# Kernel tuning notes

Hardware: AMD Instinct MI355X
Metric: run time of the kernel (lower is better)

## Reference

```python
import jax, jax.numpy as jnp
import numpy as np

N_NODES = 50000


def gcn_conv(x, row, col, W, b, n_nodes):
    # x: [N, Cin], row/col: [E+N] (self-loops already appended)
    x = x @ W  # [N, Cout]
    deg = jax.ops.segment_sum(jnp.ones(col.shape, x.dtype), col, num_segments=n_nodes)
    dinv = jnp.where(deg > 0, jax.lax.rsqrt(deg), 0.0)
    norm = dinv[row] * dinv[col]  # [E+N]
    msgs = x[row] * norm[:, None]  # gather + scale, [E+N, Cout]
    out = jax.ops.segment_sum(msgs, col, num_segments=n_nodes)
    return out + b


def setup_inputs() -> dict:
    key = jax.random.key(0)
    ks = jax.random.split(key, 5)
    n, e = N_NODES, 640000
    d_in, d_h, d_out = 128, 128, 64
    x = jax.random.normal(ks[0], (n, d_in), dtype=jnp.float32)
    edge_index = jax.random.randint(ks[1], (2, e), 0, n, dtype=jnp.int64)
    s1 = 1.0 / np.sqrt(d_in)
    s2 = 1.0 / np.sqrt(d_h)
    W1 = jax.random.normal(ks[2], (d_in, d_h), dtype=jnp.float32) * s1
    W2 = jax.random.normal(ks[3], (d_h, d_h), dtype=jnp.float32) * s2
    Wl = jax.random.normal(ks[4], (d_h, d_out), dtype=jnp.float32) * s2
    return {
        "x": x, "edge_index": edge_index,
        "W1": W1, "b1": jnp.zeros((d_h,), jnp.float32),
        "W2": W2, "b2": jnp.zeros((d_h,), jnp.float32),
        "Wl": Wl, "bl": jnp.zeros((d_out,), jnp.float32),
    }


def reference(x, edge_index, W1, b1, W2, b2, Wl, bl):
    n = x.shape[0]
    loops = jnp.arange(n, dtype=edge_index.dtype)
    row = jnp.concatenate([edge_index[0], loops])  # add self-loops (PyG GCNConv)
    col = jnp.concatenate([edge_index[1], loops])
    h = jax.nn.relu(gcn_conv(x, row, col, W1, b1, n))  # dropout is identity in eval
    h = jax.nn.relu(gcn_conv(h, row, col, W2, b2, n))
    return h @ Wl + bl
```

## Files before the change

### kernel.cpp

```cpp
#include <hip/hip_runtime.h>
#include <hip/hip_fp16.h>

#define NN 50000
#define NE 640000
#define RB ((NN + 255) / 256)

#define SC_GROUPS 8
#define SC_RANGE (NN / SC_GROUPS)
#define SC_EPT 8
#define SC_CHUNK (256 * SC_EPT)
#define SC_CHUNKS ((NE + SC_CHUNK - 1) / SC_CHUNK)

struct __align__(8) edge_t { int r; float w; };

__device__ __forceinline__ int edge_at(const void* p, long long i, int m64) {
    if (m64) return (int)((const long long*)p)[i];
    return ((const int*)p)[i];
}

__device__ __forceinline__ int detect_m64(const unsigned* w, int tid) {
    __shared__ int found;
    if (tid == 0) found = 0;
    __syncthreads();
    if (tid < 256 && w[2 * tid + 1] != 0u) atomicAdd(&found, 1);
    __syncthreads();
    return (found == 0) ? 1 : 0;
}

__global__ __launch_bounds__(256) void k_count(const void* __restrict__ e,
                                               int* __restrict__ deg) {
    int m = detect_m64((const unsigned*)e, threadIdx.x);
    int i = blockIdx.x * 256 + threadIdx.x;
    if (i >= NE) return;
    int c = edge_at(e, (long long)NE + i, m);
    if ((unsigned)c < (unsigned)NN) atomicAdd(&deg[c], 1);
}

__global__ __launch_bounds__(256) void k_reduce(const int* __restrict__ deg,
                                                int* __restrict__ bsum) {
    __shared__ int s[256];
    int i = blockIdx.x * 256 + threadIdx.x;
    s[threadIdx.x] = (i < NN) ? deg[i] : 0;
    __syncthreads();
    for (int d = 128; d > 0; d >>= 1) {
        if (threadIdx.x < d) s[threadIdx.x] += s[threadIdx.x + d];
        __syncthreads();
    }
    if (threadIdx.x == 0) bsum[blockIdx.x] = s[0];
}

__global__ __launch_bounds__(256) void k_apply(const int* __restrict__ deg,
                                               const int* __restrict__ bsum,
                                               int* __restrict__ offs,
                                               int* __restrict__ cursor,
                                               float* __restrict__ dinv) {
    __shared__ int s[256];
    __shared__ int base_s;
    int t = threadIdx.x;
    int v = (t < RB && t < blockIdx.x) ? bsum[t] : 0;
    s[t] = v;
    __syncthreads();
    for (int d = 128; d > 0; d >>= 1) {
        if (t < d) s[t] += s[t + d];
        __syncthreads();
    }
    if (t == 0) base_s = s[0];
    __syncthreads();
    int base = base_s;
    __syncthreads();
    int i = blockIdx.x * 256 + t;
    int dg = (i < NN) ? deg[i] : 0;
    s[t] = dg;
    __syncthreads();
    for (int d = 1; d < 256; d <<= 1) {
        int u = (t >= d) ? s[t - d] : 0;
        __syncthreads();
        s[t] += u;
        __syncthreads();
    }
    if (i < NN) {
        int excl = base + s[t] - dg;
        offs[i] = excl;
        cursor[i] = excl;
        dinv[i] = rsqrtf((float)(dg + 1));
        if (i == NN - 1) offs[NN] = excl + dg;
    }
}

__global__ __launch_bounds__(256) void k_scatter(const void* __restrict__ e,
                                                 int* __restrict__ cursor,
                                                 edge_t* __restrict__ ew,
                                                 const float* __restrict__ dinv) {
    int m = detect_m64((const unsigned*)e, threadIdx.x);
    int b = blockIdx.x;
    int g = b & (SC_GROUPS - 1);
    int chunk = b >> 3;
    int clo = g * SC_RANGE, chi = clo + SC_RANGE;
    int base = chunk * SC_CHUNK + threadIdx.x;
#pragma unroll
    for (int j = 0; j < SC_EPT; j++) {
        int i = base + j * 256;
        if (i < NE) {
            int c = edge_at(e, (long long)NE + i, m);
            if (c >= clo && c < chi) {
                int r = edge_at(e, (long long)i, m);
                r = min(max(r, 0), NN - 1);
                int p = atomicAdd(&cursor[c], 1);
                edge_t t2; t2.r = r; t2.w = dinv[r];
                ew[p] = t2;
            }
        }
    }
}

__global__ __launch_bounds__(256) void k_gemm128h(const float* __restrict__ A,
                                                  const float* __restrict__ W,
                                                  __half* __restrict__ Th) {
    __shared__ float Ws[64 * 128];
    int t = threadIdx.x;
    int rg = t >> 4, cg = t & 15;
    int row0 = blockIdx.x * 32 + rg * 2;
    const float4* a0 = (const float4*)(A + (long long)min(row0 + 0, NN - 1) * 128);
    const float4* a1 = (const float4*)(A + (long long)min(row0 + 1, NN - 1) * 128);
    float acc[2][8];
#pragma unroll
    for (int i = 0; i < 2; i++)
#pragma unroll
        for (int j = 0; j < 8; j++) acc[i][j] = 0.f;
#pragma unroll
    for (int h = 0; h < 2; h++) {
        __syncthreads();
#pragma unroll
        for (int i = 0; i < 8; i++)
            ((float4*)Ws)[t + 256 * i] = ((const float4*)(W + h * 64 * 128))[t + 256 * i];
        __syncthreads();
#pragma unroll 4
        for (int k4 = 0; k4 < 16; k4++) {
            float4 av0 = a0[h * 16 + k4];
            float4 av1 = a1[h * 16 + k4];
#pragma unroll
            for (int kk = 0; kk < 4; kk++) {
                float4 w0 = *(const float4*)&Ws[(k4 * 4 + kk) * 128 + cg * 4];
                float4 w1 = *(const float4*)&Ws[(k4 * 4 + kk) * 128 + cg * 4 + 64];
                float x0 = (kk == 0) ? av0.x : (kk == 1) ? av0.y : (kk == 2) ? av0.z : av0.w;
                float x1 = (kk == 0) ? av1.x : (kk == 1) ? av1.y : (kk == 2) ? av1.z : av1.w;
                acc[0][0] += x0 * w0.x; acc[0][1] += x0 * w0.y;
                acc[0][2] += x0 * w0.z; acc[0][3] += x0 * w0.w;
                acc[0][4] += x0 * w1.x; acc[0][5] += x0 * w1.y;
                acc[0][6] += x0 * w1.z; acc[0][7] += x0 * w1.w;
                acc[1][0] += x1 * w0.x; acc[1][1] += x1 * w0.y;
                acc[1][2] += x1 * w0.z; acc[1][3] += x1 * w0.w;
                acc[1][4] += x1 * w1.x; acc[1][5] += x1 * w1.y;
                acc[1][6] += x1 * w1.z; acc[1][7] += x1 * w1.w;
            }
        }
    }
#pragma unroll
    for (int i = 0; i < 2; i++) {
        int row = row0 + i;
        if (row < NN) {
            __half2 p0 = __floats2half2_rn(acc[i][0], acc[i][1]);
            __half2 p1 = __floats2half2_rn(acc[i][2], acc[i][3]);
            __half2 p2 = __floats2half2_rn(acc[i][4], acc[i][5]);
            __half2 p3 = __floats2half2_rn(acc[i][6], acc[i][7]);
            uint2 u0; u0.x = *(unsigned*)&p0; u0.y = *(unsigned*)&p1;
            uint2 u1; u1.x = *(unsigned*)&p2; u1.y = *(unsigned*)&p3;
            *(uint2*)(Th + (long long)row * 128 + cg * 4) = u0;
            *(uint2*)(Th + (long long)row * 128 + cg * 4 + 64) = u1;
        }
    }
}

__global__ __launch_bounds__(256) void k_gemm64(const float* __restrict__ A,
                                                const float* __restrict__ W,
                                                const float* __restrict__ b,
                                                float* __restrict__ T) {
    __shared__ float Ws[128 * 64];
    int t = threadIdx.x;
#pragma unroll
    for (int i = 0; i < 8; i++)
        ((float4*)Ws)[t + 256 * i] = ((const float4*)W)[t + 256 * i];
    __syncthreads();
    int rg = t >> 4, cg = t & 15;
    int row0 = blockIdx.x * 32 + rg * 2;
    const float4* a0 = (const float4*)(A + (long long)min(row0 + 0, NN - 1) * 128);
    const float4* a1 = (const float4*)(A + (long long)min(row0 + 1, NN - 1) * 128);
    float acc[2][4];
#pragma unroll
    for (int i = 0; i < 2; i++)
#pragma unroll
        for (int j = 0; j < 4; j++) acc[i][j] = 0.f;
#pragma unroll 4
    for (int k4 = 0; k4 < 32; k4++) {
        float4 av0 = a0[k4];
        float4 av1 = a1[k4];
#pragma unroll
        for (int kk = 0; kk < 4; kk++) {
            float4 w = *(const float4*)&Ws[(k4 * 4 + kk) * 64 + cg * 4];
            float x0 = (kk == 0) ? av0.x : (kk == 1) ? av0.y : (kk == 2) ? av0.z : av0.w;
            float x1 = (kk == 0) ? av1.x : (kk == 1) ? av1.y : (kk == 2) ? av1.z : av1.w;
            acc[0][0] += x0 * w.x; acc[0][1] += x0 * w.y;
            acc[0][2] += x0 * w.z; acc[0][3] += x0 * w.w;
            acc[1][0] += x1 * w.x; acc[1][1] += x1 * w.y;
            acc[1][2] += x1 * w.z; acc[1][3] += x1 * w.w;
        }
    }
    float4 bb = ((const float4*)b)[cg];
#pragma unroll
    for (int i = 0; i < 2; i++) {
        int row = row0 + i;
        if (row < NN) {
            float4 v = {acc[i][0] + bb.x, acc[i][1] + bb.y,
                        acc[i][2] + bb.z, acc[i][3] + bb.w};
            *(float4*)&T[(long long)row * 64 + cg * 4] = v;
        }
    }
}

__device__ __forceinline__ float4 h4_to_f4(uint2 u) {
    __half2 h0 = *reinterpret_cast<const __half2*>(&u.x);
    __half2 h1 = *reinterpret_cast<const __half2*>(&u.y);
    float2 f0 = __half22float2(h0);
    float2 f1 = __half22float2(h1);
    float4 r; r.x = f0.x; r.y = f0.y; r.z = f1.x; r.w = f1.y;
    return r;
}

__global__ __launch_bounds__(256) void k_agg_h(const __half* __restrict__ X,
                                               const int* __restrict__ offs,
                                               const edge_t* __restrict__ ew,
                                               const float* __restrict__ dinv,
                                               const float* __restrict__ b,
                                               float* __restrict__ H) {
    int t = threadIdx.x;
    int node = blockIdx.x * 4 + (t >> 6);
    if (node >= NN) return;
    int lane = t & 63;
    int half = lane >> 5;
    int l32 = lane & 31;
    const uint2* X2 = (const uint2*)X;
    float dc = dinv[node];
    float4 acc = {0.f, 0.f, 0.f, 0.f};
    if (half == 0) {
        float4 s = h4_to_f4(X2[(long long)node * 32 + l32]);
        acc.x = dc * s.x; acc.y = dc * s.y; acc.z = dc * s.z; acc.w = dc * s.w;
    }
    int e0 = offs[node], e1 = offs[node + 1];
    int n = e1 - e0;
    const edge_t* ep = ew + e0;
    int i = half;
    for (; i + 6 < n; i += 8) {
        edge_t m0 = ep[i], m1 = ep[i + 2], m2 = ep[i + 4], m3 = ep[i + 6];
        uint2 u0 = X2[(long long)m0.r * 32 + l32];
        uint2 u1 = X2[(long long)m1.r * 32 + l32];
        uint2 u2 = X2[(long long)m2.r * 32 + l32];
        uint2 u3 = X2[(long long)m3.r * 32 + l32];
        float4 v0 = h4_to_f4(u0), v1 = h4_to_f4(u1);
        float4 v2 = h4_to_f4(u2), v3 = h4_to_f4(u3);
        acc.x += m0.w * v0.x + m1.w * v1.x + m2.w * v2.x + m3.w * v3.x;
        acc.y += m0.w * v0.y + m1.w * v1.y + m2.w * v2.y + m3.w * v3.y;
        acc.z += m0.w * v0.z + m1.w * v1.z + m2.w * v2.z + m3.w * v3.z;
        acc.w += m0.w * v0.w + m1.w * v1.w + m2.w * v2.w + m3.w * v3.w;
    }
    for (; i < n; i += 2) {
        edge_t m = ep[i];
        float4 v = h4_to_f4(X2[(long long)m.r * 32 + l32]);
        acc.x += m.w * v.x; acc.y += m.w * v.y;
        acc.z += m.w * v.z; acc.w += m.w * v.w;
    }
    float4 oth;
    oth.x = __shfl_xor(acc.x, 32);
    oth.y = __shfl_xor(acc.y, 32);
    oth.z = __shfl_xor(acc.z, 32);
    oth.w = __shfl_xor(acc.w, 32);
    float4 bb = ((const float4*)b)[l32];
    float4 o;
    o.x = fmaxf(dc * (acc.x + oth.x) + bb.x, 0.f);
    o.y = fmaxf(dc * (acc.y + oth.y) + bb.y, 0.f);
    o.z = fmaxf(dc * (acc.z + oth.z) + bb.z, 0.f);
    o.w = fmaxf(dc * (acc.w + oth.w) + bb.w, 0.f);
    if (half == 0)
        ((float4*)H)[(long long)node * 32 + l32] = o;
}

extern "C" void kernel_launch(void* const* d_in, const int* in_sizes, int n_in,
                              void* d_out, int out_size, void* d_ws, size_t ws_size,
                              hipStream_t stream) {
    const float* x  = (const float*)d_in[0];
    const void*  ei = d_in[1];
    const float* W1 = (const float*)d_in[2];
    const float* b1 = (const float*)d_in[3];
    const float* W2 = (const float*)d_in[4];
    const float* b2 = (const float*)d_in[5];
    const float* Wl = (const float*)d_in[6];
    const float* bl = (const float*)d_in[7];
    float* out = (float*)d_out;

    char* ws = (char*)d_ws;
    size_t off = 0;
    auto alloc = [&](size_t bytes) {
        void* p = ws + off;
        off += (bytes + 255) & ~(size_t)255;
        return p;
    };
    __half* t0h    = (__half*)alloc((size_t)NN * 128 * 2);
    float*  t1     = (float*)alloc((size_t)NN * 128 * 4);
    int*    deg    = (int*)alloc((size_t)NN * 4);
    int*    offs   = (int*)alloc((size_t)(NN + 1) * 4);
    int*    cursor = (int*)alloc((size_t)NN * 4);
    edge_t* ewbuf  = (edge_t*)alloc((size_t)NE * 8);
    float*  dinv   = (float*)alloc((size_t)NN * 4);
    int*    bsum   = (int*)alloc((size_t)RB * 4);

    hipMemsetAsync(deg, 0, (size_t)NN * 4, stream);
    k_count<<<(NE + 255) / 256, 256, 0, stream>>>(ei, deg);
    k_reduce<<<RB, 256, 0, stream>>>(deg, bsum);
    k_apply<<<RB, 256, 0, stream>>>(deg, bsum, offs, cursor, dinv);
    k_scatter<<<SC_CHUNKS * SC_GROUPS, 256, 0, stream>>>(ei, cursor, ewbuf, dinv);

    int gb32 = (NN + 31) / 32;
    k_gemm128h<<<gb32, 256, 0, stream>>>(x, W1, t0h);
    k_agg_h<<<(NN + 3) / 4, 256, 0, stream>>>(t0h, offs, ewbuf, dinv, b1, t1);
    k_gemm128h<<<gb32, 256, 0, stream>>>(t1, W2, t0h);
    k_agg_h<<<(NN + 3) / 4, 256, 0, stream>>>(t0h, offs, ewbuf, dinv, b2, t1);
    k_gemm64<<<gb32, 256, 0, stream>>>(t1, Wl, bl, out);
}
```

Before: 305.6 us.

## Fuse final linear layer into second aggregation and partition degree counting

The second aggregation kernel now keeps each block's four aggregated node rows in shared memory and applies the final 128x64 linear layer plus bias directly. This removes the separate k_gemm64 launch and the round trip of the hidden activations through global memory. The degree-count kernel now uses the same chunked, node-range-partitioned scheme as the scatter kernel, so each block's atomics land in a narrower address range. The cost is that Wl is reread from global memory per block and every edge index is read 8 times in k_count. Node bounds checks were dropped, which relies on N being divisible by 4.

```diff
diff --git a/kernel.cpp b/kernel.cpp
--- a/kernel.cpp
+++ b/kernel.cpp
@@ -30,10 +30,19 @@
 __global__ __launch_bounds__(256) void k_count(const void* __restrict__ e,
                                                int* __restrict__ deg) {
     int m = detect_m64((const unsigned*)e, threadIdx.x);
-    int i = blockIdx.x * 256 + threadIdx.x;
-    if (i >= NE) return;
-    int c = edge_at(e, (long long)NE + i, m);
-    if ((unsigned)c < (unsigned)NN) atomicAdd(&deg[c], 1);
+    int b = blockIdx.x;
+    int g = b & (SC_GROUPS - 1);
+    int chunk = b >> 3;
+    int clo = g * SC_RANGE, chi = clo + SC_RANGE;
+    int base = chunk * SC_CHUNK + threadIdx.x;
+#pragma unroll
+    for (int j = 0; j < SC_EPT; j++) {
+        int i = base + j * 256;
+        if (i < NE) {
+            int c = edge_at(e, (long long)NE + i, m);
+            if (c >= clo && c < chi) atomicAdd(&deg[c], 1);
+        }
+    }
 }
 
 __global__ __launch_bounds__(256) void k_reduce(const int* __restrict__ deg,
@@ -171,52 +180,6 @@
     }
 }
 
-__global__ __launch_bounds__(256) void k_gemm64(const float* __restrict__ A,
-                                                const float* __restrict__ W,
-                                                const float* __restrict__ b,
-                                                float* __restrict__ T) {
-    __shared__ float Ws[128 * 64];
-    int t = threadIdx.x;
-#pragma unroll
-    for (int i = 0; i < 8; i++)
-        ((float4*)Ws)[t + 256 * i] = ((const float4*)W)[t + 256 * i];
-    __syncthreads();
-    int rg = t >> 4, cg = t & 15;
-    int row0 = blockIdx.x * 32 + rg * 2;
-    const float4* a0 = (const float4*)(A + (long long)min(row0 + 0, NN - 1) * 128);
-    const float4* a1 = (const float4*)(A + (long long)min(row0 + 1, NN - 1) * 128);
-    float acc[2][4];
-#pragma unroll
-    for (int i = 0; i < 2; i++)
-#pragma unroll
-        for (int j = 0; j < 4; j++) acc[i][j] = 0.f;
-#pragma unroll 4
-    for (int k4 = 0; k4 < 32; k4++) {
-        float4 av0 = a0[k4];
-        float4 av1 = a1[k4];
-#pragma unroll
-        for (int kk = 0; kk < 4; kk++) {
-            float4 w = *(const float4*)&Ws[(k4 * 4 + kk) * 64 + cg * 4];
-            float x0 = (kk == 0) ? av0.x : (kk == 1) ? av0.y : (kk == 2) ? av0.z : av0.w;
-            float x1 = (kk == 0) ? av1.x : (kk == 1) ? av1.y : (kk == 2) ? av1.z : av1.w;
-            acc[0][0] += x0 * w.x; acc[0][1] += x0 * w.y;
-            acc[0][2] += x0 * w.z; acc[0][3] += x0 * w.w;
-            acc[1][0] += x1 * w.x; acc[1][1] += x1 * w.y;
-            acc[1][2] += x1 * w.z; acc[1][3] += x1 * w.w;
-        }
-    }
-    float4 bb = ((const float4*)b)[cg];
-#pragma unroll
-    for (int i = 0; i < 2; i++) {
-        int row = row0 + i;
-        if (row < NN) {
-            float4 v = {acc[i][0] + bb.x, acc[i][1] + bb.y,
-                        acc[i][2] + bb.z, acc[i][3] + bb.w};
-            *(float4*)&T[(long long)row * 64 + cg * 4] = v;
-        }
-    }
-}
-
 __device__ __forceinline__ float4 h4_to_f4(uint2 u) {
     __half2 h0 = *reinterpret_cast<const __half2*>(&u.x);
     __half2 h1 = *reinterpret_cast<const __half2*>(&u.y);
@@ -226,20 +189,12 @@
     return r;
 }
 
-__global__ __launch_bounds__(256) void k_agg_h(const __half* __restrict__ X,
-                                               const int* __restrict__ offs,
-                                               const edge_t* __restrict__ ew,
-                                               const float* __restrict__ dinv,
-                                               const float* __restrict__ b,
-                                               float* __restrict__ H) {
-    int t = threadIdx.x;
-    int node = blockIdx.x * 4 + (t >> 6);
-    if (node >= NN) return;
-    int lane = t & 63;
-    int half = lane >> 5;
-    int l32 = lane & 31;
+__device__ __forceinline__ float4 agg_gather(const __half* __restrict__ X,
+                                             const int* __restrict__ offs,
+                                             const edge_t* __restrict__ ew,
+                                             float dc, int node, int half,
+                                             int l32, const float* __restrict__ b) {
     const uint2* X2 = (const uint2*)X;
-    float dc = dinv[node];
     float4 acc = {0.f, 0.f, 0.f, 0.f};
     if (half == 0) {
         float4 s = h4_to_f4(X2[(long long)node * 32 + l32]);
@@ -279,8 +234,64 @@
     o.y = fmaxf(dc * (acc.y + oth.y) + bb.y, 0.f);
     o.z = fmaxf(dc * (acc.z + oth.z) + bb.z, 0.f);
     o.w = fmaxf(dc * (acc.w + oth.w) + bb.w, 0.f);
+    return o;
+}
+
+__global__ __launch_bounds__(256) void k_agg_h(const __half* __restrict__ X,
+                                               const int* __restrict__ offs,
+                                               const edge_t* __restrict__ ew,
+                                               const float* __restrict__ dinv,
+                                               const float* __restrict__ b,
+                                               float* __restrict__ H) {
+    int t = threadIdx.x;
+    int node = blockIdx.x * 4 + (t >> 6);
+    int lane = t & 63;
+    int half = lane >> 5, l32 = lane & 31;
+    float dc = dinv[node];
+    float4 o = agg_gather(X, offs, ew, dc, node, half, l32, b);
     if (half == 0)
         ((float4*)H)[(long long)node * 32 + l32] = o;
+}
+
+__global__ __launch_bounds__(256) void k_agg_out(const __half* __restrict__ X,
+                                                 const int* __restrict__ offs,
+                                                 const edge_t* __restrict__ ew,
+                                                 const float* __restrict__ dinv,
+                                                 const float* __restrict__ b,
+                                                 const float* __restrict__ Wl,
+                                                 const float* __restrict__ bl,
+                                                 float* __restrict__ out) {
+    __shared__ float hs[4][128];
+    __shared__ float pacc[16][64];
+    int t = threadIdx.x;
+    int nl = t >> 6;
+    int node = blockIdx.x * 4 + nl;
+    int lane = t & 63;
+    int half = lane >> 5, l32 = lane & 31;
+    float dc = dinv[node];
+    float4 o = agg_gather(X, offs, ew, dc, node, half, l32, b);
+    if (half == 0)
+        *(float4*)&hs[nl][l32 * 4] = o;
+    __syncthreads();
+    int q = nl, j = lane;
+    float a0 = 0.f, a1 = 0.f, a2 = 0.f, a3 = 0.f;
+#pragma unroll 8
+    for (int kk = 0; kk < 32; kk++) {
+        int k = q * 32 + kk;
+        float w = Wl[k * 64 + j];
+        a0 += hs[0][k] * w;
+        a1 += hs[1][k] * w;
+        a2 += hs[2][k] * w;
+        a3 += hs[3][k] * w;
+    }
+    pacc[q * 4 + 0][j] = a0;
+    pacc[q * 4 + 1][j] = a1;
+    pacc[q * 4 + 2][j] = a2;
+    pacc[q * 4 + 3][j] = a3;
+    __syncthreads();
+    float r = pacc[0 * 4 + nl][j] + pacc[1 * 4 + nl][j]
+            + pacc[2 * 4 + nl][j] + pacc[3 * 4 + nl][j] + bl[j];
+    out[(long long)node * 64 + j] = r;
 }
 
 extern "C" void kernel_launch(void* const* d_in, const int* in_sizes, int n_in,
@@ -313,15 +324,14 @@
     int*    bsum   = (int*)alloc((size_t)RB * 4);
 
     hipMemsetAsync(deg, 0, (size_t)NN * 4, stream);
-    k_count<<<(NE + 255) / 256, 256, 0, stream>>>(ei, deg);
+    k_count<<<SC_CHUNKS * SC_GROUPS, 256, 0, stream>>>(ei, deg);
     k_reduce<<<RB, 256, 0, stream>>>(deg, bsum);
     k_apply<<<RB, 256, 0, stream>>>(deg, bsum, offs, cursor, dinv);
     k_scatter<<<SC_CHUNKS * SC_GROUPS, 256, 0, stream>>>(ei, cursor, ewbuf, dinv);
 
     int gb32 = (NN + 31) / 32;
     k_gemm128h<<<gb32, 256, 0, stream>>>(x, W1, t0h);
-    k_agg_h<<<(NN + 3) / 4, 256, 0, stream>>>(t0h, offs, ewbuf, dinv, b1, t1);
+    k_agg_h<<<NN / 4, 256, 0, stream>>>(t0h, offs, ewbuf, dinv, b1, t1);
     k_gemm128h<<<gb32, 256, 0, stream>>>(t1, W2, t0h);
-    k_agg_h<<<(NN + 3) / 4, 256, 0, stream>>>(t0h, offs, ewbuf, dinv, b2, t1);
-    k_gemm64<<<gb32, 256, 0, stream>>>(t1, Wl, bl, out);
-}
+    k_agg_out<<<NN / 4, 256, 0, stream>>>(t0h, offs, ewbuf, dinv, b2, Wl, bl, out);
+}
```

Result: no change. 305.2 us (-0.1%).

## Fuse degree counting into first GEMM launch as extra blocks

Applied to the files above, without the earlier changes.

Merges the degree-count pass and the first layer's GEMM into one launch, with extra blocks beyond the GEMM grid doing the edge counting over chunked column ranges. This lets the memory-bound atomic counting overlap the compute-bound GEMM and removes one kernel launch. Separately, the aggregation kernel drops its node bounds check and launches exactly NN/4 blocks, relying on NN being divisible by 4. The counting blocks now scan the column array once per range group, so edge reads grow by the group count.

```diff
diff --git a/kernel.cpp b/kernel.cpp
--- a/kernel.cpp
+++ b/kernel.cpp
@@ -4,6 +4,7 @@
 #define NN 50000
 #define NE 640000
 #define RB ((NN + 255) / 256)
+#define GB32 ((NN + 31) / 32)
 
 #define SC_GROUPS 8
 #define SC_RANGE (NN / SC_GROUPS)
@@ -27,97 +28,30 @@
     return (found == 0) ? 1 : 0;
 }
 
-__global__ __launch_bounds__(256) void k_count(const void* __restrict__ e,
-                                               int* __restrict__ deg) {
-    int m = detect_m64((const unsigned*)e, threadIdx.x);
-    int i = blockIdx.x * 256 + threadIdx.x;
-    if (i >= NE) return;
-    int c = edge_at(e, (long long)NE + i, m);
-    if ((unsigned)c < (unsigned)NN) atomicAdd(&deg[c], 1);
-}
-
-__global__ __launch_bounds__(256) void k_reduce(const int* __restrict__ deg,
-                                                int* __restrict__ bsum) {
-    __shared__ int s[256];
-    int i = blockIdx.x * 256 + threadIdx.x;
-    s[threadIdx.x] = (i < NN) ? deg[i] : 0;
-    __syncthreads();
-    for (int d = 128; d > 0; d >>= 1) {
-        if (threadIdx.x < d) s[threadIdx.x] += s[threadIdx.x + d];
-        __syncthreads();
-    }
-    if (threadIdx.x == 0) bsum[blockIdx.x] = s[0];
-}
-
-__global__ __launch_bounds__(256) void k_apply(const int* __restrict__ deg,
-                                               const int* __restrict__ bsum,
-                                               int* __restrict__ offs,
-                                               int* __restrict__ cursor,
-                                               float* __restrict__ dinv) {
-    __shared__ int s[256];
-    __shared__ int base_s;
-    int t = threadIdx.x;
-    int v = (t < RB && t < blockIdx.x) ? bsum[t] : 0;
-    s[t] = v;
-    __syncthreads();
-    for (int d = 128; d > 0; d >>= 1) {
-        if (t < d) s[t] += s[t + d];
-        __syncthreads();
-    }
-    if (t == 0) base_s = s[0];
-    __syncthreads();
-    int base = base_s;
-    __syncthreads();
-    int i = blockIdx.x * 256 + t;
-    int dg = (i < NN) ? deg[i] : 0;
-    s[t] = dg;
-    __syncthreads();
-    for (int d = 1; d < 256; d <<= 1) {
-        int u = (t >= d) ? s[t - d] : 0;
-        __syncthreads();
-        s[t] += u;
-        __syncthreads();
-    }
-    if (i < NN) {
-        int excl = base + s[t] - dg;
-        offs[i] = excl;
-        cursor[i] = excl;
-        dinv[i] = rsqrtf((float)(dg + 1));
-        if (i == NN - 1) offs[NN] = excl + dg;
-    }
-}
-
-__global__ __launch_bounds__(256) void k_scatter(const void* __restrict__ e,
-                                                 int* __restrict__ cursor,
-                                                 edge_t* __restrict__ ew,
-                                                 const float* __restrict__ dinv) {
-    int m = detect_m64((const unsigned*)e, threadIdx.x);
-    int b = blockIdx.x;
-    int g = b & (SC_GROUPS - 1);
-    int chunk = b >> 3;
-    int clo = g * SC_RANGE, chi = clo + SC_RANGE;
-    int base = chunk * SC_CHUNK + threadIdx.x;
-#pragma unroll
-    for (int j = 0; j < SC_EPT; j++) {
-        int i = base + j * 256;
-        if (i < NE) {
-            int c = edge_at(e, (long long)NE + i, m);
-            if (c >= clo && c < chi) {
-                int r = edge_at(e, (long long)i, m);
-                r = min(max(r, 0), NN - 1);
-                int p = atomicAdd(&cursor[c], 1);
-                edge_t t2; t2.r = r; t2.w = dinv[r];
-                ew[p] = t2;
+__global__ __launch_bounds__(256) void k_count_gemm(const void* __restrict__ e,
+                                                    int* __restrict__ deg,
+                                                    const float* __restrict__ A,
+                                                    const float* __restrict__ W,
+                                                    __half* __restrict__ Th) {
+    __shared__ float Ws[64 * 128];
+    int t = threadIdx.x;
+    if (blockIdx.x >= GB32) {
+        int m = detect_m64((const unsigned*)e, t);
+        int b = blockIdx.x - GB32;
+        int g = b & (SC_GROUPS - 1);
+        int chunk = b >> 3;
+        int clo = g * SC_RANGE, chi = clo + SC_RANGE;
+        int base = chunk * SC_CHUNK + t;
+#pragma unroll
+        for (int j = 0; j < SC_EPT; j++) {
+            int i = base + j * 256;
+            if (i < NE) {
+                int c = edge_at(e, (long long)NE + i, m);
+                if (c >= clo && c < chi) atomicAdd(&deg[c], 1);
             }
         }
-    }
-}
-
-__global__ __launch_bounds__(256) void k_gemm128h(const float* __restrict__ A,
-                                                  const float* __restrict__ W,
-                                                  __half* __restrict__ Th) {
-    __shared__ float Ws[64 * 128];
-    int t = threadIdx.x;
+        return;
+    }
     int rg = t >> 4, cg = t & 15;
     int row0 = blockIdx.x * 32 + rg * 2;
     const float4* a0 = (const float4*)(A + (long long)min(row0 + 0, NN - 1) * 128);
@@ -171,6 +105,141 @@
     }
 }
 
+__global__ __launch_bounds__(256) void k_reduce(const int* __restrict__ deg,
+                                                int* __restrict__ bsum) {
+    __shared__ int s[256];
+    int i = blockIdx.x * 256 + threadIdx.x;
+    s[threadIdx.x] = (i < NN) ? deg[i] : 0;
+    __syncthreads();
+    for (int d = 128; d > 0; d >>= 1) {
+        if (threadIdx.x < d) s[threadIdx.x] += s[threadIdx.x + d];
+        __syncthreads();
+    }
+    if (threadIdx.x == 0) bsum[blockIdx.x] = s[0];
+}
+
+__global__ __launch_bounds__(256) void k_apply(const int* __restrict__ deg,
+                                               const int* __restrict__ bsum,
+                                               int* __restrict__ offs,
+                                               int* __restrict__ cursor,
+                                               float* __restrict__ dinv) {
+    __shared__ int s[256];
+    __shared__ int base_s;
+    int t = threadIdx.x;
+    int v = (t < RB && t < blockIdx.x) ? bsum[t] : 0;
+    s[t] = v;
+    __syncthreads();
+    for (int d = 128; d > 0; d >>= 1) {
+        if (t < d) s[t] += s[t + d];
+        __syncthreads();
+    }
+    if (t == 0) base_s = s[0];
+    __syncthreads();
+    int base = base_s;
+    __syncthreads();
+    int i = blockIdx.x * 256 + t;
+    int dg = (i < NN) ? deg[i] : 0;
+    s[t] = dg;
+    __syncthreads();
+    for (int d = 1; d < 256; d <<= 1) {
+        int u = (t >= d) ? s[t - d] : 0;
+        __syncthreads();
+        s[t] += u;
+        __syncthreads();
+    }
+    if (i < NN) {
+        int excl = base + s[t] - dg;
+        offs[i] = excl;
+        cursor[i] = excl;
+        dinv[i] = rsqrtf((float)(dg + 1));
+        if (i == NN - 1) offs[NN] = excl + dg;
+    }
+}
+
+__global__ __launch_bounds__(256) void k_scatter(const void* __restrict__ e,
+                                                 int* __restrict__ cursor,
+                                                 edge_t* __restrict__ ew,
+                                                 const float* __restrict__ dinv) {
+    int m = detect_m64((const unsigned*)e, threadIdx.x);
+    int b = blockIdx.x;
+    int g = b & (SC_GROUPS - 1);
+    int chunk = b >> 3;
+    int clo = g * SC_RANGE, chi = clo + SC_RANGE;
+    int base = chunk * SC_CHUNK + threadIdx.x;
+#pragma unroll
+    for (int j = 0; j < SC_EPT; j++) {
+        int i = base + j * 256;
+        if (i < NE) {
+            int c = edge_at(e, (long long)NE + i, m);
+            if (c >= clo && c < chi) {
+                int r = edge_at(e, (long long)i, m);
+                r = min(max(r, 0), NN - 1);
+                int p = atomicAdd(&cursor[c], 1);
+                edge_t t2; t2.r = r; t2.w = dinv[r];
+                ew[p] = t2;
+            }
+        }
+    }
+}
+
+__global__ __launch_bounds__(256) void k_gemm128h(const float* __restrict__ A,
+                                                  const float* __restrict__ W,
+                                                  __half* __restrict__ Th) {
+    __shared__ float Ws[64 * 128];
+    int t = threadIdx.x;
+    int rg = t >> 4, cg = t & 15;
+    int row0 = blockIdx.x * 32 + rg * 2;
+    const float4* a0 = (const float4*)(A + (long long)min(row0 + 0, NN - 1) * 128);
+    const float4* a1 = (const float4*)(A + (long long)min(row0 + 1, NN - 1) * 128);
+    float acc[2][8];
+#pragma unroll
+    for (int i = 0; i < 2; i++)
+#pragma unroll
+        for (int j = 0; j < 8; j++) acc[i][j] = 0.f;
+#pragma unroll
+    for (int h = 0; h < 2; h++) {
+        __syncthreads();
+#pragma unroll
+        for (int i = 0; i < 8; i++)
+            ((float4*)Ws)[t + 256 * i] = ((const float4*)(W + h * 64 * 128))[t + 256 * i];
+        __syncthreads();
+#pragma unroll 4
+        for (int k4 = 0; k4 < 16; k4++) {
+            float4 av0 = a0[h * 16 + k4];
+            float4 av1 = a1[h * 16 + k4];
+#pragma unroll
+            for (int kk = 0; kk < 4; kk++) {
+                float4 w0 = *(const float4*)&Ws[(k4 * 4 + kk) * 128 + cg * 4];
+                float4 w1 = *(const float4*)&Ws[(k4 * 4 + kk) * 128 + cg * 4 + 64];
+                float x0 = (kk == 0) ? av0.x : (kk == 1) ? av0.y : (kk == 2) ? av0.z : av0.w;
+                float x1 = (kk == 0) ? av1.x : (kk == 1) ? av1.y : (kk == 2) ? av1.z : av1.w;
+                acc[0][0] += x0 * w0.x; acc[0][1] += x0 * w0.y;
+                acc[0][2] += x0 * w0.z; acc[0][3] += x0 * w0.w;
+                acc[0][4] += x0 * w1.x; acc[0][5] += x0 * w1.y;
+                acc[0][6] += x0 * w1.z; acc[0][7] += x0 * w1.w;
+                acc[1][0] += x1 * w0.x; acc[1][1] += x1 * w0.y;
+                acc[1][2] += x1 * w0.z; acc[1][3] += x1 * w0.w;
+                acc[1][4] += x1 * w1.x; acc[1][5] += x1 * w1.y;
+                acc[1][6] += x1 * w1.z; acc[1][7] += x1 * w1.w;
+            }
+        }
+    }
+#pragma unroll
+    for (int i = 0; i < 2; i++) {
+        int row = row0 + i;
+        if (row < NN) {
+            __half2 p0 = __floats2half2_rn(acc[i][0], acc[i][1]);
+            __half2 p1 = __floats2half2_rn(acc[i][2], acc[i][3]);
+            __half2 p2 = __floats2half2_rn(acc[i][4], acc[i][5]);
+            __half2 p3 = __floats2half2_rn(acc[i][6], acc[i][7]);
+            uint2 u0; u0.x = *(unsigned*)&p0; u0.y = *(unsigned*)&p1;
+            uint2 u1; u1.x = *(unsigned*)&p2; u1.y = *(unsigned*)&p3;
+            *(uint2*)(Th + (long long)row * 128 + cg * 4) = u0;
+            *(uint2*)(Th + (long long)row * 128 + cg * 4 + 64) = u1;
+        }
+    }
+}
+
 __global__ __launch_bounds__(256) void k_gemm64(const float* __restrict__ A,
                                                 const float* __restrict__ W,
                                                 const float* __restrict__ b,
@@ -234,10 +303,8 @@
                                                float* __restrict__ H) {
     int t = threadIdx.x;
     int node = blockIdx.x * 4 + (t >> 6);
-    if (node >= NN) return;
     int lane = t & 63;
-    int half = lane >> 5;
-    int l32 = lane & 31;
+    int half = lane >> 5, l32 = lane & 31;
     const uint2* X2 = (const uint2*)X;
     float dc = dinv[node];
     float4 acc = {0.f, 0.f, 0.f, 0.f};
@@ -313,15 +380,13 @@
     int*    bsum   = (int*)alloc((size_t)RB * 4);
 
     hipMemsetAsync(deg, 0, (size_t)NN * 4, stream);
-    k_count<<<(NE + 255) / 256, 256, 0, stream>>>(ei, deg);
+    k_count_gemm<<<GB32 + SC_CHUNKS * SC_GROUPS, 256, 0, stream>>>(ei, deg, x, W1, t0h);
     k_reduce<<<RB, 256, 0, stream>>>(deg, bsum);
     k_apply<<<RB, 256, 0, stream>>>(deg, bsum, offs, cursor, dinv);
     k_scatter<<<SC_CHUNKS * SC_GROUPS, 256, 0, stream>>>(ei, cursor, ewbuf, dinv);
 
-    int gb32 = (NN + 31) / 32;
-    k_gemm128h<<<gb32, 256, 0, stream>>>(x, W1, t0h);
-    k_agg_h<<<(NN + 3) / 4, 256, 0, stream>>>(t0h, offs, ewbuf, dinv, b1, t1);
-    k_gemm128h<<<gb32, 256, 0, stream>>>(t1, W2, t0h);
-    k_agg_h<<<(NN + 3) / 4, 256, 0, stream>>>(t0h, offs, ewbuf, dinv, b2, t1);
-    k_gemm64<<<gb32, 256, 0, stream>>>(t1, Wl, bl, out);
-}
+    k_agg_h<<<NN / 4, 256, 0, stream>>>(t0h, offs, ewbuf, dinv, b1, t1);
+    k_gemm128h<<<GB32, 256, 0, stream>>>(t1, W2, t0h);
+    k_agg_h<<<NN / 4, 256, 0, stream>>>(t0h, offs, ewbuf, dinv, b2, t1);
+    k_gemm64<<<GB32, 256, 0, stream>>>(t1, Wl, bl, out);
+}
```

After: 294.2 us. -3.7%, faster.

## Co-schedule first GEMM halves with edge count and scatter kernels

Applied to the files above, without the earlier changes.

Splits the first feature GEMM into two halves and fuses each into the same launch as the degree-count and CSR-scatter kernels, with block-index partitioning. Independent work now shares the GPU, filling the idle time of the latency-bound atomic passes and cutting two launches. GEMM weight tiles in LDS shrink (32-row and 64-row chunks) so more blocks fit per CU, at the cost of extra syncthreads. The node bound check in aggregation is dropped because NN is divisible by 4.

```diff
diff --git a/kernel.cpp b/kernel.cpp
--- a/kernel.cpp
+++ b/kernel.cpp
@@ -4,6 +4,10 @@
 #define NN 50000
 #define NE 640000
 #define RB ((NN + 255) / 256)
+
+#define GA_BLOCKS 781
+#define GB_BLOCKS 782
+#define GB32 ((NN + 31) / 32)
 
 #define SC_GROUPS 8
 #define SC_RANGE (NN / SC_GROUPS)
@@ -27,99 +31,12 @@
     return (found == 0) ? 1 : 0;
 }
 
-__global__ __launch_bounds__(256) void k_count(const void* __restrict__ e,
-                                               int* __restrict__ deg) {
-    int m = detect_m64((const unsigned*)e, threadIdx.x);
-    int i = blockIdx.x * 256 + threadIdx.x;
-    if (i >= NE) return;
-    int c = edge_at(e, (long long)NE + i, m);
-    if ((unsigned)c < (unsigned)NN) atomicAdd(&deg[c], 1);
-}
-
-__global__ __launch_bounds__(256) void k_reduce(const int* __restrict__ deg,
-                                                int* __restrict__ bsum) {
-    __shared__ int s[256];
-    int i = blockIdx.x * 256 + threadIdx.x;
-    s[threadIdx.x] = (i < NN) ? deg[i] : 0;
-    __syncthreads();
-    for (int d = 128; d > 0; d >>= 1) {
-        if (threadIdx.x < d) s[threadIdx.x] += s[threadIdx.x + d];
-        __syncthreads();
-    }
-    if (threadIdx.x == 0) bsum[blockIdx.x] = s[0];
-}
-
-__global__ __launch_bounds__(256) void k_apply(const int* __restrict__ deg,
-                                               const int* __restrict__ bsum,
-                                               int* __restrict__ offs,
-                                               int* __restrict__ cursor,
-                                               float* __restrict__ dinv) {
-    __shared__ int s[256];
-    __shared__ int base_s;
-    int t = threadIdx.x;
-    int v = (t < RB && t < blockIdx.x) ? bsum[t] : 0;
-    s[t] = v;
-    __syncthreads();
-    for (int d = 128; d > 0; d >>= 1) {
-        if (t < d) s[t] += s[t + d];
-        __syncthreads();
-    }
-    if (t == 0) base_s = s[0];
-    __syncthreads();
-    int base = base_s;
-    __syncthreads();
-    int i = blockIdx.x * 256 + t;
-    int dg = (i < NN) ? deg[i] : 0;
-    s[t] = dg;
-    __syncthreads();
-    for (int d = 1; d < 256; d <<= 1) {
-        int u = (t >= d) ? s[t - d] : 0;
-        __syncthreads();
-        s[t] += u;
-        __syncthreads();
-    }
-    if (i < NN) {
-        int excl = base + s[t] - dg;
-        offs[i] = excl;
-        cursor[i] = excl;
-        dinv[i] = rsqrtf((float)(dg + 1));
-        if (i == NN - 1) offs[NN] = excl + dg;
-    }
-}
-
-__global__ __launch_bounds__(256) void k_scatter(const void* __restrict__ e,
-                                                 int* __restrict__ cursor,
-                                                 edge_t* __restrict__ ew,
-                                                 const float* __restrict__ dinv) {
-    int m = detect_m64((const unsigned*)e, threadIdx.x);
-    int b = blockIdx.x;
-    int g = b & (SC_GROUPS - 1);
-    int chunk = b >> 3;
-    int clo = g * SC_RANGE, chi = clo + SC_RANGE;
-    int base = chunk * SC_CHUNK + threadIdx.x;
-#pragma unroll
-    for (int j = 0; j < SC_EPT; j++) {
-        int i = base + j * 256;
-        if (i < NE) {
-            int c = edge_at(e, (long long)NE + i, m);
-            if (c >= clo && c < chi) {
-                int r = edge_at(e, (long long)i, m);
-                r = min(max(r, 0), NN - 1);
-                int p = atomicAdd(&cursor[c], 1);
-                edge_t t2; t2.r = r; t2.w = dinv[r];
-                ew[p] = t2;
-            }
-        }
-    }
-}
-
-__global__ __launch_bounds__(256) void k_gemm128h(const float* __restrict__ A,
-                                                  const float* __restrict__ W,
-                                                  __half* __restrict__ Th) {
-    __shared__ float Ws[64 * 128];
-    int t = threadIdx.x;
+__device__ __forceinline__ void gemm32_body(const float* __restrict__ A,
+                                            const float* __restrict__ W,
+                                            __half* __restrict__ Th,
+                                            int row0_blk, int t, float* Ws) {
     int rg = t >> 4, cg = t & 15;
-    int row0 = blockIdx.x * 32 + rg * 2;
+    int row0 = row0_blk + rg * 2;
     const float4* a0 = (const float4*)(A + (long long)min(row0 + 0, NN - 1) * 128);
     const float4* a1 = (const float4*)(A + (long long)min(row0 + 1, NN - 1) * 128);
     float acc[2][8];
@@ -128,16 +45,16 @@
 #pragma unroll
         for (int j = 0; j < 8; j++) acc[i][j] = 0.f;
 #pragma unroll
-    for (int h = 0; h < 2; h++) {
-        __syncthreads();
-#pragma unroll
-        for (int i = 0; i < 8; i++)
-            ((float4*)Ws)[t + 256 * i] = ((const float4*)(W + h * 64 * 128))[t + 256 * i];
+    for (int h = 0; h < 4; h++) {
+        __syncthreads();
+#pragma unroll
+        for (int i = 0; i < 4; i++)
+            ((float4*)Ws)[t + 256 * i] = ((const float4*)(W + h * 32 * 128))[t + 256 * i];
         __syncthreads();
 #pragma unroll 4
-        for (int k4 = 0; k4 < 16; k4++) {
-            float4 av0 = a0[h * 16 + k4];
-            float4 av1 = a1[h * 16 + k4];
+        for (int k4 = 0; k4 < 8; k4++) {
+            float4 av0 = a0[h * 8 + k4];
+            float4 av1 = a1[h * 8 + k4];
 #pragma unroll
             for (int kk = 0; kk < 4; kk++) {
                 float4 w0 = *(const float4*)&Ws[(k4 * 4 + kk) * 128 + cg * 4];
@@ -171,16 +88,132 @@
     }
 }
 
+__global__ __launch_bounds__(256) void k_gemm_count(const void* __restrict__ e,
+                                                    int* __restrict__ deg,
+                                                    const float* __restrict__ A,
+                                                    const float* __restrict__ W,
+                                                    __half* __restrict__ Th) {
+    __shared__ float Ws[32 * 128];
+    int t = threadIdx.x;
+    if (blockIdx.x >= GA_BLOCKS) {
+        int m = detect_m64((const unsigned*)e, t);
+        int b = blockIdx.x - GA_BLOCKS;
+        int g = b & (SC_GROUPS - 1);
+        int chunk = b >> 3;
+        int clo = g * SC_RANGE, chi = clo + SC_RANGE;
+        int base = chunk * SC_CHUNK + t;
+#pragma unroll
+        for (int j = 0; j < SC_EPT; j++) {
+            int i = base + j * 256;
+            if (i < NE) {
+                int c = edge_at(e, (long long)NE + i, m);
+                if (c >= clo && c < chi) atomicAdd(&deg[c], 1);
+            }
+        }
+        return;
+    }
+    gemm32_body(A, W, Th, blockIdx.x * 32, t, Ws);
+}
+
+__global__ __launch_bounds__(256) void k_gemm_scatter(const void* __restrict__ e,
+                                                      int* __restrict__ cursor,
+                                                      edge_t* __restrict__ ew,
+                                                      const float* __restrict__ dinv,
+                                                      const float* __restrict__ A,
+                                                      const float* __restrict__ W,
+                                                      __half* __restrict__ Th) {
+    __shared__ float Ws[32 * 128];
+    int t = threadIdx.x;
+    if (blockIdx.x >= GB_BLOCKS) {
+        int m = detect_m64((const unsigned*)e, t);
+        int b = blockIdx.x - GB_BLOCKS;
+        int g = b & (SC_GROUPS - 1);
+        int chunk = b >> 3;
+        int clo = g * SC_RANGE, chi = clo + SC_RANGE;
+        int base = chunk * SC_CHUNK + t;
+#pragma unroll
+        for (int j = 0; j < SC_EPT; j++) {
+            int i = base + j * 256;
+            if (i < NE) {
+                int c = edge_at(e, (long long)NE + i, m);
+                if (c >= clo && c < chi) {
+                    int r = edge_at(e, (long long)i, m);
+                    r = min(max(r, 0), NN - 1);
+                    int p = atomicAdd(&cursor[c], 1);
+                    edge_t t2; t2.r = r; t2.w = dinv[r];
+                    ew[p] = t2;
+                }
+            }
+        }
+        return;
+    }
+    gemm32_body(A, W, Th, (GA_BLOCKS + blockIdx.x) * 32, t, Ws);
+}
+
+__global__ __launch_bounds__(256) void k_reduce(const int* __restrict__ deg,
+                                                int* __restrict__ bsum) {
+    __shared__ int s[256];
+    int i = blockIdx.x * 256 + threadIdx.x;
+    s[threadIdx.x] = (i < NN) ? deg[i] : 0;
+    __syncthreads();
+    for (int d = 128; d > 0; d >>= 1) {
+        if (threadIdx.x < d) s[threadIdx.x] += s[threadIdx.x + d];
+        __syncthreads();
+    }
+    if (threadIdx.x == 0) bsum[blockIdx.x] = s[0];
+}
+
+__global__ __launch_bounds__(256) void k_apply(const int* __restrict__ deg,
+                                               const int* __restrict__ bsum,
+                                               int* __restrict__ offs,
+                                               int* __restrict__ cursor,
+                                               float* __restrict__ dinv) {
+    __shared__ int s[256];
+    __shared__ int base_s;
+    int t = threadIdx.x;
+    int v = (t < RB && t < blockIdx.x) ? bsum[t] : 0;
+    s[t] = v;
+    __syncthreads();
+    for (int d = 128; d > 0; d >>= 1) {
+        if (t < d) s[t] += s[t + d];
+        __syncthreads();
+    }
+    if (t == 0) base_s = s[0];
+    __syncthreads();
+    int base = base_s;
+    __syncthreads();
+    int i = blockIdx.x * 256 + t;
+    int dg = (i < NN) ? deg[i] : 0;
+    s[t] = dg;
+    __syncthreads();
+    for (int d = 1; d < 256; d <<= 1) {
+        int u = (t >= d) ? s[t - d] : 0;
+        __syncthreads();
+        s[t] += u;
+        __syncthreads();
+    }
+    if (i < NN) {
+        int excl = base + s[t] - dg;
+        offs[i] = excl;
+        cursor[i] = excl;
+        dinv[i] = rsqrtf((float)(dg + 1));
+        if (i == NN - 1) offs[NN] = excl + dg;
+    }
+}
+
+__global__ __launch_bounds__(256) void k_gemm128h(const float* __restrict__ A,
+                                                  const float* __restrict__ W,
+                                                  __half* __restrict__ Th) {
+    __shared__ float Ws[32 * 128];
+    gemm32_body(A, W, Th, blockIdx.x * 32, threadIdx.x, Ws);
+}
+
 __global__ __launch_bounds__(256) void k_gemm64(const float* __restrict__ A,
                                                 const float* __restrict__ W,
                                                 const float* __restrict__ b,
                                                 float* __restrict__ T) {
-    __shared__ float Ws[128 * 64];
-    int t = threadIdx.x;
-#pragma unroll
-    for (int i = 0; i < 8; i++)
-        ((float4*)Ws)[t + 256 * i] = ((const float4*)W)[t + 256 * i];
-    __syncthreads();
+    __shared__ float Ws[64 * 64];
+    int t = threadIdx.x;
     int rg = t >> 4, cg = t & 15;
     int row0 = blockIdx.x * 32 + rg * 2;
     const float4* a0 = (const float4*)(A + (long long)min(row0 + 0, NN - 1) * 128);
@@ -190,19 +223,27 @@
     for (int i = 0; i < 2; i++)
 #pragma unroll
         for (int j = 0; j < 4; j++) acc[i][j] = 0.f;
+#pragma unroll
+    for (int h = 0; h < 2; h++) {
+        __syncthreads();
+#pragma unroll
+        for (int i = 0; i < 4; i++)
+            ((float4*)Ws)[t + 256 * i] = ((const float4*)(W + h * 64 * 64))[t + 256 * i];
+        __syncthreads();
 #pragma unroll 4
-    for (int k4 = 0; k4 < 32; k4++) {
-        float4 av0 = a0[k4];
-        float4 av1 = a1[k4];
-#pragma unroll
-        for (int kk = 0; kk < 4; kk++) {
-            float4 w = *(const float4*)&Ws[(k4 * 4 + kk) * 64 + cg * 4];
-            float x0 = (kk == 0) ? av0.x : (kk == 1) ? av0.y : (kk == 2) ? av0.z : av0.w;
-            float x1 = (kk == 0) ? av1.x : (kk == 1) ? av1.y : (kk == 2) ? av1.z : av1.w;
-            acc[0][0] += x0 * w.x; acc[0][1] += x0 * w.y;
-            acc[0][2] += x0 * w.z; acc[0][3] += x0 * w.w;
-            acc[1][0] += x1 * w.x; acc[1][1] += x1 * w.y;
-            acc[1][2] += x1 * w.z; acc[1][3] += x1 * w.w;
+        for (int k4 = 0; k4 < 16; k4++) {
+            float4 av0 = a0[h * 16 + k4];
+            float4 av1 = a1[h * 16 + k4];
+#pragma unroll
+            for (int kk = 0; kk < 4; kk++) {
+                float4 w = *(const float4*)&Ws[(k4 * 4 + kk) * 64 + cg * 4];
+                float x0 = (kk == 0) ? av0.x : (kk == 1) ? av0.y : (kk == 2) ? av0.z : av0.w;
+                float x1 = (kk == 0) ? av1.x : (kk == 1) ? av1.y : (kk == 2) ? av1.z : av1.w;
+                acc[0][0] += x0 * w.x; acc[0][1] += x0 * w.y;
+                acc[0][2] += x0 * w.z; acc[0][3] += x0 * w.w;
+                acc[1][0] += x1 * w.x; acc[1][1] += x1 * w.y;
+                acc[1][2] += x1 * w.z; acc[1][3] += x1 * w.w;
+            }
         }
     }
     float4 bb = ((const float4*)b)[cg];
@@ -234,10 +275,8 @@
                                                float* __restrict__ H) {
     int t = threadIdx.x;
     int node = blockIdx.x * 4 + (t >> 6);
-    if (node >= NN) return;
     int lane = t & 63;
-    int half = lane >> 5;
-    int l32 = lane & 31;
+    int half = lane >> 5, l32 = lane & 31;
     const uint2* X2 = (const uint2*)X;
     float dc = dinv[node];
     float4 acc = {0.f, 0.f, 0.f, 0.f};
@@ -313,15 +352,14 @@
     int*    bsum   = (int*)alloc((size_t)RB * 4);
 
     hipMemsetAsync(deg, 0, (size_t)NN * 4, stream);
-    k_count<<<(NE + 255) / 256, 256, 0, stream>>>(ei, deg);
+    k_gemm_count<<<GA_BLOCKS + SC_CHUNKS * SC_GROUPS, 256, 0, stream>>>(ei, deg, x, W1, t0h);
     k_reduce<<<RB, 256, 0, stream>>>(deg, bsum);
     k_apply<<<RB, 256, 0, stream>>>(deg, bsum, offs, cursor, dinv);
-    k_scatter<<<SC_CHUNKS * SC_GROUPS, 256, 0, stream>>>(ei, cursor, ewbuf, dinv);
-
-    int gb32 = (NN + 31) / 32;
-    k_gemm128h<<<gb32, 256, 0, stream>>>(x, W1, t0h);
-    k_agg_h<<<(NN + 3) / 4, 256, 0, stream>>>(t0h, offs, ewbuf, dinv, b1, t1);
-    k_gemm128h<<<gb32, 256, 0, stream>>>(t1, W2, t0h);
-    k_agg_h<<<(NN + 3) / 4, 256, 0, stream>>>(t0h, offs, ewbuf, dinv, b2, t1);
-    k_gemm64<<<gb32, 256, 0, stream>>>(t1, Wl, bl, out);
-}
+    k_gemm_scatter<<<GB_BLOCKS + SC_CHUNKS * SC_GROUPS, 256, 0, stream>>>(
+        ei, cursor, ewbuf, dinv, x, W1, t0h);
+
+    k_agg_h<<<NN / 4, 256, 0, stream>>>(t0h, offs, ewbuf, dinv, b1, t1);
+    k_gemm128h<<<GB32, 256, 0, stream>>>(t1, W2, t0h);
+    k_agg_h<<<NN / 4, 256, 0, stream>>>(t0h, offs, ewbuf, dinv, b2, t1);
+    k_gemm64<<<GB32, 256, 0, stream>>>(t1, Wl, bl, out);
+}
```

Result: faster. 296.4 us (-3.0%).
